# Optimization experiments

Hardware: AMD Instinct MI355X
Metric: run time of the kernel (lower is better)

The kernel has to match this reference:

```python
import jax, jax.numpy as jnp
import numpy as np

B, T, SD, AD, H, K, HID = 256, 128, 8, 2, 3, 4, 256


def setup_inputs() -> dict:
    key = jax.random.key(0)
    ks = jax.random.split(key, 12)
    inp = {
        "state": jax.random.normal(ks[0], (B, T, SD), dtype=jnp.float32),
        "action": jax.random.normal(ks[1], (B, T, AD), dtype=jnp.float32),
        # Linear(4, 4*H, bias=False): weight (4*H, 4)
        "Wk": jax.random.normal(ks[2], (4 * H, K), dtype=jnp.float32) * 0.1,
        "Wq": jax.random.normal(ks[3], (4 * H, SD + AD), dtype=jnp.float32) * 0.1,
        "Wv": jax.random.normal(ks[4], (4 * H, K), dtype=jnp.float32) * 0.1,
        # MLP: in_dim = 4*H + SD + AD -> HID -> HID -> 1
        "W1": jax.random.normal(ks[5], (HID, 4 * H + SD + AD), dtype=jnp.float32) * 0.05,
        "b1": jnp.zeros((HID,), dtype=jnp.float32),
        "W2": jax.random.normal(ks[6], (HID, HID), dtype=jnp.float32) * 0.05,
        "b2": jnp.zeros((HID,), dtype=jnp.float32),
        "Wout": jax.random.uniform(ks[7], (1, HID), minval=-0.003, maxval=0.003, dtype=jnp.float32),
        "bout": jax.random.uniform(ks[8], (1,), minval=-0.003, maxval=0.003, dtype=jnp.float32),
    }
    return inp


def reference(state, action, Wk, Wq, Wv, W1, b1, W2, b2, Wout, bout):
    q_state = jnp.concatenate([state, action], axis=-1)  # (b, t, sd+ad)
    s = state[:, :, :4]                                   # (b, t, 4)
    b, t, k = s.shape
    h = Wk.shape[0] // k
    # rel_full[b, i, j] = s[b, j] - s[b, i]  (matches torch view/transpose)
    rel_full = s[:, None, :, :] - s[:, :, None, :]        # (b, t, t, 4)
    # drop diagonal (self-pairs): idx[i] = all j != i, in order
    j = jnp.arange(t - 1)
    idx = j[None, :] + (j[None, :] >= jnp.arange(t)[:, None])  # (t, t-1)
    rel = jnp.take_along_axis(rel_full, idx[None, :, :, None], axis=2)  # (b, t, t-1, 4)
    # QKV projections (tiny head dim k=4)
    q = (q_state @ Wq.T).reshape(b, t, h, k)              # (b, t, h, 4)
    keys = (rel @ Wk.T).reshape(b, t, t - 1, h, k)        # (b, t, t-1, h, 4)
    vals = (rel @ Wv.T).reshape(b, t, t - 1, h, k)
    scores = jnp.einsum('bthk,btjhk->bthj', q, keys) / jnp.sqrt(jnp.float32(k))
    w = jax.nn.softmax(scores, axis=-1)                   # over the t-1 neighbors
    x = jnp.einsum('bthj,btjhk->bthk', w, vals).reshape(b, t, h * k)
    x = jnp.concatenate([x, q_state], axis=-1)            # (b, t, h*4 + sd+ad)
    x = jax.nn.relu(x @ W1.T + b1)
    x = jax.nn.relu(x @ W2.T + b2)
    return x @ Wout.T + bout                              # (b, t, 1)
```

## Files before the change

### kernel.cpp

```cpp
#include <hip/hip_runtime.h>
#include <math.h>

#define Bp 256
#define Tp 128
#define SDp 8
#define ADp 2
#define Hp 3
#define Kp 4
#define HIDp 256
#define QDp (SDp + ADp)
#define X1Dp (Hp * Kp + QDp)
#define X1PAD 32
#define H1LD 264
#define LOG2E 1.4426950408889634f

typedef short bf16x8 __attribute__((ext_vector_type(8)));
typedef float f32x4  __attribute__((ext_vector_type(4)));

__device__ __forceinline__ unsigned short f2bf(float f) {
    unsigned u = __float_as_uint(f);
    unsigned r = (u + 0x7FFFu + ((u >> 16) & 1u)) >> 16;
    return (unsigned short)r;
}

__global__ __launch_bounds__(256) void attn_prep_kernel(
    const float* __restrict__ state, const float* __restrict__ action,
    const float* __restrict__ Wk, const float* __restrict__ Wq,
    const float* __restrict__ Wv, const float* __restrict__ W1,
    const float* __restrict__ W2, unsigned short* __restrict__ W1b,
    unsigned short* __restrict__ W2b, unsigned short* __restrict__ X1b)
{
    if (blockIdx.x >= Bp) {
        const int id0 = (blockIdx.x - Bp) * 1024 + threadIdx.x * 4;
        if (id0 < HIDp * HIDp) {
            const float4 v = *(const float4*)(W2 + id0);
            ushort4 o;
            o.x = f2bf(v.x); o.y = f2bf(v.y); o.z = f2bf(v.z); o.w = f2bf(v.w);
            *(ushort4*)(W2b + id0) = o;
        } else {
            #pragma unroll
            for (int u = 0; u < 4; ++u) {
                const int i = id0 - HIDp * HIDp + u;
                const int r = i >> 5, k = i & 31;
                W1b[i] = (k < X1Dp) ? f2bf(W1[r * X1Dp + k]) : (unsigned short)0;
            }
        }
        return;
    }

    const int b  = blockIdx.x;
    const int t  = threadIdx.x & 127;
    const int jh = threadIdx.x >> 7;

    __shared__ float4 s4[Tp];
    __shared__ float  wq[Hp * Kp * QDp];
    __shared__ float  wk[Hp * Kp * Kp];
    __shared__ float  wv[Hp * Kp * Kp];
    __shared__ float  part[Tp][16];

    if (threadIdx.x < Tp)
        s4[threadIdx.x] = ((const float4*)(state + (size_t)b * Tp * SDp))[threadIdx.x * 2];
    if (threadIdx.x >= Tp && threadIdx.x < Tp + Hp * Kp * QDp)
        wq[threadIdx.x - Tp] = Wq[threadIdx.x - Tp];
    if (threadIdx.x < Hp * Kp * Kp) { wk[threadIdx.x] = Wk[threadIdx.x]; wv[threadIdx.x] = Wv[threadIdx.x]; }
    __syncthreads();

    float qs[QDp];
    {
        const float* srow = state + ((size_t)b * Tp + t) * SDp;
        #pragma unroll
        for (int d = 0; d < SDp; ++d) qs[d] = srow[d];
        const float* arow = action + ((size_t)b * Tp + t) * ADp;
        qs[8] = arow[0]; qs[9] = arow[1];
    }

    float q[Hp * Kp];
    #pragma unroll
    for (int r = 0; r < Hp * Kp; ++r) {
        float a = 0.f;
        #pragma unroll
        for (int d = 0; d < QDp; ++d) a += qs[d] * wq[r * QDp + d];
        q[r] = a;
    }
    float qkp[Hp * Kp];
    #pragma unroll
    for (int h = 0; h < Hp; ++h)
        #pragma unroll
        for (int c = 0; c < Kp; ++c) {
            float a = 0.f;
            #pragma unroll
            for (int k = 0; k < Kp; ++k) a += q[h * Kp + k] * wk[(h * Kp + k) * Kp + c];
            qkp[h * Kp + c] = 0.5f * LOG2E * a;
        }

    const float4 st = s4[t];
    float ch[Hp];
    #pragma unroll
    for (int h = 0; h < Hp; ++h)
        ch[h] = st.x * qkp[h*4] + st.y * qkp[h*4+1] + st.z * qkp[h*4+2] + st.w * qkp[h*4+3];

    float l[Hp] = {0.f, 0.f, 0.f};
    float accs[Hp][4] = {};
    const int j0 = jh * 64;
    for (int j = j0; j < j0 + 64; ++j) {
        const float4 sj = s4[j];
        #pragma unroll
        for (int h = 0; h < Hp; ++h) {
            const float d = sj.x * qkp[h*4] + sj.y * qkp[h*4+1]
                          + sj.z * qkp[h*4+2] + sj.w * qkp[h*4+3] - ch[h];
            const float e = (j == t) ? 0.f : exp2f(d);
            l[h] += e;
            accs[h][0] += e * sj.x; accs[h][1] += e * sj.y;
            accs[h][2] += e * sj.z; accs[h][3] += e * sj.w;
        }
    }

    if (jh == 1) {
        #pragma unroll
        for (int h = 0; h < Hp; ++h) {
            part[t][h] = l[h];
            #pragma unroll
            for (int c = 0; c < Kp; ++c) part[t][3 + h * 4 + c] = accs[h][c];
        }
    }
    __syncthreads();

    if (jh == 0) {
        unsigned short rowb[X1PAD];
        #pragma unroll
        for (int h = 0; h < Hp; ++h) {
            const float lt = l[h] + part[t][h];
            const float inv = 1.f / lt;
            const float rb0 = (accs[h][0] + part[t][3 + h*4 + 0]) * inv - st.x;
            const float rb1 = (accs[h][1] + part[t][3 + h*4 + 1]) * inv - st.y;
            const float rb2 = (accs[h][2] + part[t][3 + h*4 + 2]) * inv - st.z;
            const float rb3 = (accs[h][3] + part[t][3 + h*4 + 3]) * inv - st.w;
            #pragma unroll
            for (int k = 0; k < Kp; ++k) {
                const int r = h * Kp + k;
                rowb[r] = f2bf(rb0 * wv[r*4] + rb1 * wv[r*4+1] + rb2 * wv[r*4+2] + rb3 * wv[r*4+3]);
            }
        }
        #pragma unroll
        for (int i = 0; i < QDp; ++i) rowb[Hp * Kp + i] = f2bf(qs[i]);
        #pragma unroll
        for (int i = X1Dp; i < X1PAD; ++i) rowb[i] = 0;

        uint4* dst = (uint4*)(X1b + ((size_t)b * Tp + t) * X1PAD);
        const uint4* srcv = (const uint4*)rowb;
        #pragma unroll
        for (int i = 0; i < 4; ++i) dst[i] = srcv[i];
    }
}

__global__ __launch_bounds__(256, 4) void mlp_kernel(
    const unsigned short* __restrict__ X1b, const unsigned short* __restrict__ W1b,
    const unsigned short* __restrict__ W2b,
    const float* __restrict__ b1, const float* __restrict__ b2,
    const float* __restrict__ Wout, const float* __restrict__ bout,
    float* __restrict__ out)
{
    const int tid  = threadIdx.x;
    const int lane = tid & 63;
    const int wave = tid >> 6;
    const int quad = lane >> 4;
    const int l16  = lane & 15;
    const int pos0 = blockIdx.x * 64;

    __shared__ __align__(16) unsigned short h1s[64 * H1LD];

    {
        const bf16x8 afr = *(const bf16x8*)&X1b[((size_t)pos0 + wave * 16 + l16) * X1PAD + quad * 8];
        for (int nt = 0; nt < 16; ++nt) {
            const bf16x8 bfr = *(const bf16x8*)&W1b[(nt * 16 + l16) * X1PAD + quad * 8];
            f32x4 acc = {0.f, 0.f, 0.f, 0.f};
            acc = __builtin_amdgcn_mfma_f32_16x16x32_bf16(afr, bfr, acc, 0, 0, 0);
            const int col = nt * 16 + l16;
            const float bb = b1[col];
            #pragma unroll
            for (int r = 0; r < 4; ++r)
                h1s[(wave * 16 + quad * 4 + r) * H1LD + col] = f2bf(fmaxf(acc[r] + bb, 0.f));
        }
    }
    __syncthreads();

    bf16x8 A[8];
    #pragma unroll
    for (int ks = 0; ks < 8; ++ks)
        A[ks] = *(const bf16x8*)&h1s[(wave * 16 + l16) * H1LD + ks * 32 + quad * 8];

    float rsum[4] = {0.f, 0.f, 0.f, 0.f};
    for (int nt = 0; nt < 16; ++nt) {
        const int col = nt * 16 + l16;
        const unsigned short* wrow = W2b + (size_t)col * HIDp + quad * 8;
        bf16x8 Bf[8];
        #pragma unroll
        for (int ks = 0; ks < 8; ++ks)
            Bf[ks] = *(const bf16x8*)(wrow + ks * 32);
        f32x4 acc = {0.f, 0.f, 0.f, 0.f};
        #pragma unroll
        for (int ks = 0; ks < 8; ++ks)
            acc = __builtin_amdgcn_mfma_f32_16x16x32_bf16(A[ks], Bf[ks], acc, 0, 0, 0);
        const float bb = b2[col];
        const float wo = Wout[col];
        #pragma unroll
        for (int r = 0; r < 4; ++r)
            rsum[r] += fmaxf(acc[r] + bb, 0.f) * wo;
    }

    #pragma unroll
    for (int off = 1; off < 16; off <<= 1)
        #pragma unroll
        for (int r = 0; r < 4; ++r)
            rsum[r] += __shfl_xor(rsum[r], off, 64);

    if (l16 == 0) {
        const float bo = bout[0];
        #pragma unroll
        for (int r = 0; r < 4; ++r)
            out[pos0 + wave * 16 + quad * 4 + r] = rsum[r] + bo;
    }
}

extern "C" void kernel_launch(void* const* d_in, const int* in_sizes, int n_in,
                              void* d_out, int out_size, void* d_ws, size_t ws_size,
                              hipStream_t stream) {
    const float* state  = (const float*)d_in[0];
    const float* action = (const float*)d_in[1];
    const float* Wk     = (const float*)d_in[2];
    const float* Wq     = (const float*)d_in[3];
    const float* Wv     = (const float*)d_in[4];
    const float* W1     = (const float*)d_in[5];
    const float* b1     = (const float*)d_in[6];
    const float* W2     = (const float*)d_in[7];
    const float* b2     = (const float*)d_in[8];
    const float* Wout   = (const float*)d_in[9];
    const float* bout   = (const float*)d_in[10];
    float* out = (float*)d_out;

    char* ws = (char*)d_ws;
    unsigned short* W1b = (unsigned short*)(ws);
    unsigned short* W2b = (unsigned short*)(ws + 16384);
    unsigned short* X1b = (unsigned short*)(ws + 16384 + 131072);

    attn_prep_kernel<<<Bp + 72, 256, 0, stream>>>(state, action, Wk, Wq, Wv, W1, W2,
                                                  W1b, W2b, X1b);
    mlp_kernel<<<(Bp * Tp) / 64, 256, 0, stream>>>(X1b, W1b, W2b, b1, b2, Wout, bout, out);
}
```

Measured before the change: 121.0 us.

## Fuse attention prep and MLP into one kernel with LDS-staged weights

Merges the attention-prep and MLP kernels into a single 512-thread kernel, one block per batch element. The attention output and the bf16 W1 now stay in LDS instead of going through a global workspace, and the neighbour loop is split across four thread groups instead of two. Each block converts W2 to bf16 and stages it through LDS in two halves, replacing the per-wave global loads of W2. The cost is redundant W2 conversion in every block and about 135KB of LDS per block, which limits occupancy to one block per CU.

```diff
diff --git a/kernel.cpp b/kernel.cpp
--- a/kernel.cpp
+++ b/kernel.cpp
@@ -10,7 +10,8 @@
 #define HIDp 256
 #define QDp (SDp + ADp)
 #define X1Dp (Hp * Kp + QDp)
-#define X1PAD 32
+#define X1LD 40
+#define W1LD 40
 #define H1LD 264
 #define LOG2E 1.4426950408889634f
 
@@ -23,46 +24,53 @@
     return (unsigned short)r;
 }
 
-__global__ __launch_bounds__(256) void attn_prep_kernel(
+__global__ __launch_bounds__(512, 2) void fused_kernel(
     const float* __restrict__ state, const float* __restrict__ action,
     const float* __restrict__ Wk, const float* __restrict__ Wq,
     const float* __restrict__ Wv, const float* __restrict__ W1,
-    const float* __restrict__ W2, unsigned short* __restrict__ W1b,
-    unsigned short* __restrict__ W2b, unsigned short* __restrict__ X1b)
+    const float* __restrict__ b1, const float* __restrict__ W2,
+    const float* __restrict__ b2, const float* __restrict__ Wout,
+    const float* __restrict__ bout, float* __restrict__ out)
 {
-    if (blockIdx.x >= Bp) {
-        const int id0 = (blockIdx.x - Bp) * 1024 + threadIdx.x * 4;
-        if (id0 < HIDp * HIDp) {
-            const float4 v = *(const float4*)(W2 + id0);
-            ushort4 o;
-            o.x = f2bf(v.x); o.y = f2bf(v.y); o.z = f2bf(v.z); o.w = f2bf(v.w);
-            *(ushort4*)(W2b + id0) = o;
-        } else {
-            #pragma unroll
-            for (int u = 0; u < 4; ++u) {
-                const int i = id0 - HIDp * HIDp + u;
-                const int r = i >> 5, k = i & 31;
-                W1b[i] = (k < X1Dp) ? f2bf(W1[r * X1Dp + k]) : (unsigned short)0;
-            }
-        }
-        return;
-    }
-
-    const int b  = blockIdx.x;
-    const int t  = threadIdx.x & 127;
-    const int jh = threadIdx.x >> 7;
-
-    __shared__ float4 s4[Tp];
-    __shared__ float  wq[Hp * Kp * QDp];
-    __shared__ float  wk[Hp * Kp * Kp];
-    __shared__ float  wv[Hp * Kp * Kp];
-    __shared__ float  part[Tp][16];
-
-    if (threadIdx.x < Tp)
-        s4[threadIdx.x] = ((const float4*)(state + (size_t)b * Tp * SDp))[threadIdx.x * 2];
-    if (threadIdx.x >= Tp && threadIdx.x < Tp + Hp * Kp * QDp)
-        wq[threadIdx.x - Tp] = Wq[threadIdx.x - Tp];
-    if (threadIdx.x < Hp * Kp * Kp) { wk[threadIdx.x] = Wk[threadIdx.x]; wv[threadIdx.x] = Wv[threadIdx.x]; }
+    __shared__ __align__(16) char lds[135168];
+    unsigned short* h1s = (unsigned short*)lds;
+    char* R2 = lds + 67584;
+    float*  part = (float*)(R2);
+    float4* s4   = (float4*)(R2 + 26112);
+    float*  wq   = (float*)(R2 + 28160);
+    float*  wk   = (float*)(R2 + 28640);
+    float*  wv   = (float*)(R2 + 28832);
+    unsigned short* W1s = (unsigned short*)(R2 + 29024);
+    unsigned short* X1s = (unsigned short*)(R2 + 49504);
+    unsigned short* W2s = (unsigned short*)(R2);
+
+    const int b    = blockIdx.x;
+    const int tid  = threadIdx.x;
+    const int t    = tid & 127;
+    const int jh   = tid >> 7;
+    const int lane = tid & 63;
+    const int wave = tid >> 6;
+    const int quad = lane >> 4;
+    const int l16  = lane & 15;
+
+    if (tid < Tp) {
+        s4[tid] = ((const float4*)(state + (size_t)b * Tp * SDp))[tid * 2];
+    } else if (tid < Tp + 120) {
+        wq[tid - Tp] = Wq[tid - Tp];
+    } else if (tid < Tp + 168) {
+        wk[tid - Tp - 120] = Wk[tid - Tp - 120];
+    } else if (tid < Tp + 216) {
+        wv[tid - Tp - 168] = Wv[tid - Tp - 168];
+    }
+    {
+        const int row = tid >> 1, c0 = (tid & 1) * 16;
+        const float* wr = W1 + row * X1Dp;
+        #pragma unroll
+        for (int i = 0; i < 16; ++i) {
+            const int c = c0 + i;
+            W1s[row * W1LD + c] = (c < X1Dp) ? f2bf(wr[c]) : (unsigned short)0;
+        }
+    }
     __syncthreads();
 
     float qs[QDp];
@@ -94,20 +102,20 @@
         }
 
     const float4 st = s4[t];
-    float ch[Hp];
+    float ch0[Hp];
     #pragma unroll
     for (int h = 0; h < Hp; ++h)
-        ch[h] = st.x * qkp[h*4] + st.y * qkp[h*4+1] + st.z * qkp[h*4+2] + st.w * qkp[h*4+3];
+        ch0[h] = st.x * qkp[h*4] + st.y * qkp[h*4+1] + st.z * qkp[h*4+2] + st.w * qkp[h*4+3];
 
     float l[Hp] = {0.f, 0.f, 0.f};
     float accs[Hp][4] = {};
-    const int j0 = jh * 64;
-    for (int j = j0; j < j0 + 64; ++j) {
+    const int j0 = jh * 32;
+    for (int j = j0; j < j0 + 32; ++j) {
         const float4 sj = s4[j];
         #pragma unroll
         for (int h = 0; h < Hp; ++h) {
             const float d = sj.x * qkp[h*4] + sj.y * qkp[h*4+1]
-                          + sj.z * qkp[h*4+2] + sj.w * qkp[h*4+3] - ch[h];
+                          + sj.z * qkp[h*4+2] + sj.w * qkp[h*4+3] - ch0[h];
             const float e = (j == t) ? 0.f : exp2f(d);
             l[h] += e;
             accs[h][0] += e * sj.x; accs[h][1] += e * sj.y;
@@ -115,26 +123,35 @@
         }
     }
 
-    if (jh == 1) {
+    if (jh > 0) {
+        float* pp = part + ((jh - 1) * 128 + t) * 17;
         #pragma unroll
         for (int h = 0; h < Hp; ++h) {
-            part[t][h] = l[h];
-            #pragma unroll
-            for (int c = 0; c < Kp; ++c) part[t][3 + h * 4 + c] = accs[h][c];
+            pp[h] = l[h];
+            #pragma unroll
+            for (int c = 0; c < Kp; ++c) pp[3 + h * 4 + c] = accs[h][c];
         }
     }
     __syncthreads();
 
     if (jh == 0) {
-        unsigned short rowb[X1PAD];
+        unsigned short rowb[32] __attribute__((aligned(16)));
         #pragma unroll
         for (int h = 0; h < Hp; ++h) {
-            const float lt = l[h] + part[t][h];
+            float lt = l[h];
+            float a0 = accs[h][0], a1 = accs[h][1], a2 = accs[h][2], a3 = accs[h][3];
+            #pragma unroll
+            for (int p = 0; p < 3; ++p) {
+                const float* pp = part + (p * 128 + t) * 17;
+                lt += pp[h];
+                a0 += pp[3 + h*4 + 0]; a1 += pp[3 + h*4 + 1];
+                a2 += pp[3 + h*4 + 2]; a3 += pp[3 + h*4 + 3];
+            }
             const float inv = 1.f / lt;
-            const float rb0 = (accs[h][0] + part[t][3 + h*4 + 0]) * inv - st.x;
-            const float rb1 = (accs[h][1] + part[t][3 + h*4 + 1]) * inv - st.y;
-            const float rb2 = (accs[h][2] + part[t][3 + h*4 + 2]) * inv - st.z;
-            const float rb3 = (accs[h][3] + part[t][3 + h*4 + 3]) * inv - st.w;
+            const float rb0 = a0 * inv - st.x;
+            const float rb1 = a1 * inv - st.y;
+            const float rb2 = a2 * inv - st.z;
+            const float rb3 = a3 * inv - st.w;
             #pragma unroll
             for (int k = 0; k < Kp; ++k) {
                 const int r = h * Kp + k;
@@ -144,35 +161,19 @@
         #pragma unroll
         for (int i = 0; i < QDp; ++i) rowb[Hp * Kp + i] = f2bf(qs[i]);
         #pragma unroll
-        for (int i = X1Dp; i < X1PAD; ++i) rowb[i] = 0;
-
-        uint4* dst = (uint4*)(X1b + ((size_t)b * Tp + t) * X1PAD);
+        for (int i = X1Dp; i < 32; ++i) rowb[i] = 0;
+
+        uint4* dst = (uint4*)(X1s + t * X1LD);
         const uint4* srcv = (const uint4*)rowb;
         #pragma unroll
         for (int i = 0; i < 4; ++i) dst[i] = srcv[i];
     }
-}
-
-__global__ __launch_bounds__(256, 4) void mlp_kernel(
-    const unsigned short* __restrict__ X1b, const unsigned short* __restrict__ W1b,
-    const unsigned short* __restrict__ W2b,
-    const float* __restrict__ b1, const float* __restrict__ b2,
-    const float* __restrict__ Wout, const float* __restrict__ bout,
-    float* __restrict__ out)
-{
-    const int tid  = threadIdx.x;
-    const int lane = tid & 63;
-    const int wave = tid >> 6;
-    const int quad = lane >> 4;
-    const int l16  = lane & 15;
-    const int pos0 = blockIdx.x * 64;
-
-    __shared__ __align__(16) unsigned short h1s[64 * H1LD];
+    __syncthreads();
 
     {
-        const bf16x8 afr = *(const bf16x8*)&X1b[((size_t)pos0 + wave * 16 + l16) * X1PAD + quad * 8];
+        const bf16x8 afr = *(const bf16x8*)&X1s[(wave * 16 + l16) * X1LD + quad * 8];
         for (int nt = 0; nt < 16; ++nt) {
-            const bf16x8 bfr = *(const bf16x8*)&W1b[(nt * 16 + l16) * X1PAD + quad * 8];
+            const bf16x8 bfr = *(const bf16x8*)&W1s[(nt * 16 + l16) * W1LD + quad * 8];
             f32x4 acc = {0.f, 0.f, 0.f, 0.f};
             acc = __builtin_amdgcn_mfma_f32_16x16x32_bf16(afr, bfr, acc, 0, 0, 0);
             const int col = nt * 16 + l16;
@@ -190,22 +191,36 @@
         A[ks] = *(const bf16x8*)&h1s[(wave * 16 + l16) * H1LD + ks * 32 + quad * 8];
 
     float rsum[4] = {0.f, 0.f, 0.f, 0.f};
-    for (int nt = 0; nt < 16; ++nt) {
-        const int col = nt * 16 + l16;
-        const unsigned short* wrow = W2b + (size_t)col * HIDp + quad * 8;
-        bf16x8 Bf[8];
-        #pragma unroll
-        for (int ks = 0; ks < 8; ++ks)
-            Bf[ks] = *(const bf16x8*)(wrow + ks * 32);
-        f32x4 acc = {0.f, 0.f, 0.f, 0.f};
-        #pragma unroll
-        for (int ks = 0; ks < 8; ++ks)
-            acc = __builtin_amdgcn_mfma_f32_16x16x32_bf16(A[ks], Bf[ks], acc, 0, 0, 0);
-        const float bb = b2[col];
-        const float wo = Wout[col];
-        #pragma unroll
-        for (int r = 0; r < 4; ++r)
-            rsum[r] += fmaxf(acc[r] + bb, 0.f) * wo;
+    const int srow8 = tid >> 6;
+    const int c4    = tid & 63;
+    #pragma unroll
+    for (int chh = 0; chh < 2; ++chh) {
+        if (chh) __syncthreads();
+        #pragma unroll
+        for (int pass = 0; pass < 16; ++pass) {
+            const int r_loc = pass * 8 + srow8;
+            const float4 v = *(const float4*)(W2 + ((size_t)(chh * 128 + r_loc)) * HIDp + c4 * 4);
+            ushort4 o;
+            o.x = f2bf(v.x); o.y = f2bf(v.y); o.z = f2bf(v.z); o.w = f2bf(v.w);
+            *(ushort4*)&W2s[r_loc * H1LD + c4 * 4] = o;
+        }
+        __syncthreads();
+        for (int nt = 0; nt < 8; ++nt) {
+            const int col = chh * 128 + nt * 16 + l16;
+            bf16x8 Bf[8];
+            #pragma unroll
+            for (int ks = 0; ks < 8; ++ks)
+                Bf[ks] = *(const bf16x8*)&W2s[(nt * 16 + l16) * H1LD + ks * 32 + quad * 8];
+            f32x4 acc = {0.f, 0.f, 0.f, 0.f};
+            #pragma unroll
+            for (int ks = 0; ks < 8; ++ks)
+                acc = __builtin_amdgcn_mfma_f32_16x16x32_bf16(A[ks], Bf[ks], acc, 0, 0, 0);
+            const float bb = b2[col];
+            const float wo = Wout[col];
+            #pragma unroll
+            for (int r = 0; r < 4; ++r)
+                rsum[r] += fmaxf(acc[r] + bb, 0.f) * wo;
+        }
     }
 
     #pragma unroll
@@ -218,7 +233,7 @@
         const float bo = bout[0];
         #pragma unroll
         for (int r = 0; r < 4; ++r)
-            out[pos0 + wave * 16 + quad * 4 + r] = rsum[r] + bo;
+            out[(size_t)b * Tp + wave * 16 + quad * 4 + r] = rsum[r] + bo;
     }
 }
 
@@ -238,12 +253,8 @@
     const float* bout   = (const float*)d_in[10];
     float* out = (float*)d_out;
 
-    char* ws = (char*)d_ws;
-    unsigned short* W1b = (unsigned short*)(ws);
-    unsigned short* W2b = (unsigned short*)(ws + 16384);
-    unsigned short* X1b = (unsigned short*)(ws + 16384 + 131072);
-
-    attn_prep_kernel<<<Bp + 72, 256, 0, stream>>>(state, action, Wk, Wq, Wv, W1, W2,
-                                                  W1b, W2b, X1b);
-    mlp_kernel<<<(Bp * Tp) / 64, 256, 0, stream>>>(X1b, W1b, W2b, b1, b2, Wout, bout, out);
+    (void)d_ws; (void)ws_size;
+
+    fused_kernel<<<Bp, 512, 0, stream>>>(state, action, Wk, Wq, Wv, W1, b1,
+                                         W2, b2, Wout, bout, out);
 }
```

Result: faster. 114.5 us (-5.4%).

## Fuse attention and MLP into one kernel with XOR-swizzled LDS and N-split layer two

Applied to the files above, without the earlier changes.

Merges the attention and MLP kernels so X1 stays in LDS and never goes through global memory. Weight conversion moves into a separate small prep kernel. Each block now handles 64 positions of one batch row, with the 128-key loop split across the four quads and combined by shuffles. Layer two is split by output columns per wave, so each W2 tile loaded from global is reused across four row tiles. The h1 buffer uses an XOR swizzle to avoid LDS bank conflicts. The cost is more registers (A[4][8]), fewer blocks (512), and the attention phase now running in the same kernel as the MFMA work.

```diff
diff --git a/kernel.cpp b/kernel.cpp
--- a/kernel.cpp
+++ b/kernel.cpp
@@ -10,8 +10,7 @@
 #define HIDp 256
 #define QDp (SDp + ADp)
 #define X1Dp (Hp * Kp + QDp)
-#define X1PAD 32
-#define H1LD 264
+#define X1LD 40
 #define LOG2E 1.4426950408889634f
 
 typedef short bf16x8 __attribute__((ext_vector_type(8)));
@@ -23,54 +22,70 @@
     return (unsigned short)r;
 }
 
-__global__ __launch_bounds__(256) void attn_prep_kernel(
+__device__ __forceinline__ unsigned h1_byte(int row, int col2bytes) {
+    unsigned off = ((unsigned)row << 9) + (unsigned)col2bytes;
+    return off ^ ((unsigned)(row & 7) << 4);
+}
+
+__global__ __launch_bounds__(256) void prep_kernel(
+    const float* __restrict__ W1, const float* __restrict__ W2,
+    unsigned short* __restrict__ W1b, unsigned short* __restrict__ W2b)
+{
+    const int bid = blockIdx.x;
+    if (bid < 64) {
+        const int i = (bid * 256 + threadIdx.x) * 4;
+        const float4 v = *(const float4*)(W2 + i);
+        ushort4 o;
+        o.x = f2bf(v.x); o.y = f2bf(v.y); o.z = f2bf(v.z); o.w = f2bf(v.w);
+        *(ushort4*)(W2b + i) = o;
+    } else {
+        const int i = (bid - 64) * 256 + threadIdx.x;
+        const int r = i >> 5, c = i & 31;
+        W1b[i] = (c < X1Dp) ? f2bf(W1[r * X1Dp + c]) : (unsigned short)0;
+    }
+}
+
+__global__ __launch_bounds__(256, 2) void main_kernel(
     const float* __restrict__ state, const float* __restrict__ action,
     const float* __restrict__ Wk, const float* __restrict__ Wq,
-    const float* __restrict__ Wv, const float* __restrict__ W1,
-    const float* __restrict__ W2, unsigned short* __restrict__ W1b,
-    unsigned short* __restrict__ W2b, unsigned short* __restrict__ X1b)
+    const float* __restrict__ Wv,
+    const unsigned short* __restrict__ W1b, const unsigned short* __restrict__ W2b,
+    const float* __restrict__ b1, const float* __restrict__ b2,
+    const float* __restrict__ Wout, const float* __restrict__ bout,
+    float* __restrict__ out)
 {
-    if (blockIdx.x >= Bp) {
-        const int id0 = (blockIdx.x - Bp) * 1024 + threadIdx.x * 4;
-        if (id0 < HIDp * HIDp) {
-            const float4 v = *(const float4*)(W2 + id0);
-            ushort4 o;
-            o.x = f2bf(v.x); o.y = f2bf(v.y); o.z = f2bf(v.z); o.w = f2bf(v.w);
-            *(ushort4*)(W2b + id0) = o;
-        } else {
-            #pragma unroll
-            for (int u = 0; u < 4; ++u) {
-                const int i = id0 - HIDp * HIDp + u;
-                const int r = i >> 5, k = i & 31;
-                W1b[i] = (k < X1Dp) ? f2bf(W1[r * X1Dp + k]) : (unsigned short)0;
-            }
-        }
-        return;
-    }
-
-    const int b  = blockIdx.x;
-    const int t  = threadIdx.x & 127;
-    const int jh = threadIdx.x >> 7;
+    const int bid   = blockIdx.x;
+    const int batch = bid >> 1;
+    const int t0    = (bid & 1) * 64;
+    const int tid   = threadIdx.x;
+    const int lane  = tid & 63;
+    const int wave  = tid >> 6;
+    const int l16   = lane & 15;
+    const int quad  = lane >> 4;
+    const int pos   = wave * 16 + l16;
+    const int t     = t0 + pos;
 
     __shared__ float4 s4[Tp];
     __shared__ float  wq[Hp * Kp * QDp];
     __shared__ float  wk[Hp * Kp * Kp];
     __shared__ float  wv[Hp * Kp * Kp];
-    __shared__ float  part[Tp][16];
-
-    if (threadIdx.x < Tp)
-        s4[threadIdx.x] = ((const float4*)(state + (size_t)b * Tp * SDp))[threadIdx.x * 2];
-    if (threadIdx.x >= Tp && threadIdx.x < Tp + Hp * Kp * QDp)
-        wq[threadIdx.x - Tp] = Wq[threadIdx.x - Tp];
-    if (threadIdx.x < Hp * Kp * Kp) { wk[threadIdx.x] = Wk[threadIdx.x]; wv[threadIdx.x] = Wv[threadIdx.x]; }
+    __shared__ __align__(16) unsigned short X1s[64 * X1LD];
+    __shared__ __align__(16) unsigned short h1s[64 * 256];
+    __shared__ __align__(16) float partial[4][64];
+
+    if (tid < Tp)
+        s4[tid] = ((const float4*)(state + (size_t)batch * Tp * SDp))[tid * 2];
+    if (tid >= Tp && tid < Tp + Hp * Kp * QDp)
+        wq[tid - Tp] = Wq[tid - Tp];
+    if (tid < Hp * Kp * Kp) { wk[tid] = Wk[tid]; wv[tid] = Wv[tid]; }
     __syncthreads();
 
     float qs[QDp];
     {
-        const float* srow = state + ((size_t)b * Tp + t) * SDp;
+        const float* srow = state + ((size_t)batch * Tp + t) * SDp;
         #pragma unroll
         for (int d = 0; d < SDp; ++d) qs[d] = srow[d];
-        const float* arow = action + ((size_t)b * Tp + t) * ADp;
+        const float* arow = action + ((size_t)batch * Tp + t) * ADp;
         qs[8] = arow[0]; qs[9] = arow[1];
     }
 
@@ -94,131 +109,138 @@
         }
 
     const float4 st = s4[t];
-    float ch[Hp];
+    float ch0[Hp];
     #pragma unroll
     for (int h = 0; h < Hp; ++h)
-        ch[h] = st.x * qkp[h*4] + st.y * qkp[h*4+1] + st.z * qkp[h*4+2] + st.w * qkp[h*4+3];
+        ch0[h] = st.x * qkp[h*4] + st.y * qkp[h*4+1] + st.z * qkp[h*4+2] + st.w * qkp[h*4+3];
 
     float l[Hp] = {0.f, 0.f, 0.f};
     float accs[Hp][4] = {};
-    const int j0 = jh * 64;
-    for (int j = j0; j < j0 + 64; ++j) {
+    const int j0 = quad * 32;
+    for (int j = j0; j < j0 + 32; ++j) {
         const float4 sj = s4[j];
         #pragma unroll
         for (int h = 0; h < Hp; ++h) {
             const float d = sj.x * qkp[h*4] + sj.y * qkp[h*4+1]
-                          + sj.z * qkp[h*4+2] + sj.w * qkp[h*4+3] - ch[h];
+                          + sj.z * qkp[h*4+2] + sj.w * qkp[h*4+3] - ch0[h];
             const float e = (j == t) ? 0.f : exp2f(d);
             l[h] += e;
             accs[h][0] += e * sj.x; accs[h][1] += e * sj.y;
             accs[h][2] += e * sj.z; accs[h][3] += e * sj.w;
         }
     }
-
-    if (jh == 1) {
-        #pragma unroll
-        for (int h = 0; h < Hp; ++h) {
-            part[t][h] = l[h];
-            #pragma unroll
-            for (int c = 0; c < Kp; ++c) part[t][3 + h * 4 + c] = accs[h][c];
-        }
-    }
-    __syncthreads();
-
-    if (jh == 0) {
-        unsigned short rowb[X1PAD];
-        #pragma unroll
-        for (int h = 0; h < Hp; ++h) {
-            const float lt = l[h] + part[t][h];
-            const float inv = 1.f / lt;
-            const float rb0 = (accs[h][0] + part[t][3 + h*4 + 0]) * inv - st.x;
-            const float rb1 = (accs[h][1] + part[t][3 + h*4 + 1]) * inv - st.y;
-            const float rb2 = (accs[h][2] + part[t][3 + h*4 + 2]) * inv - st.z;
-            const float rb3 = (accs[h][3] + part[t][3 + h*4 + 3]) * inv - st.w;
-            #pragma unroll
-            for (int k = 0; k < Kp; ++k) {
-                const int r = h * Kp + k;
-                rowb[r] = f2bf(rb0 * wv[r*4] + rb1 * wv[r*4+1] + rb2 * wv[r*4+2] + rb3 * wv[r*4+3]);
-            }
-        }
-        #pragma unroll
-        for (int i = 0; i < QDp; ++i) rowb[Hp * Kp + i] = f2bf(qs[i]);
-        #pragma unroll
-        for (int i = X1Dp; i < X1PAD; ++i) rowb[i] = 0;
-
-        uint4* dst = (uint4*)(X1b + ((size_t)b * Tp + t) * X1PAD);
-        const uint4* srcv = (const uint4*)rowb;
-        #pragma unroll
-        for (int i = 0; i < 4; ++i) dst[i] = srcv[i];
-    }
-}
-
-__global__ __launch_bounds__(256, 4) void mlp_kernel(
-    const unsigned short* __restrict__ X1b, const unsigned short* __restrict__ W1b,
-    const unsigned short* __restrict__ W2b,
-    const float* __restrict__ b1, const float* __restrict__ b2,
-    const float* __restrict__ Wout, const float* __restrict__ bout,
-    float* __restrict__ out)
-{
-    const int tid  = threadIdx.x;
-    const int lane = tid & 63;
-    const int wave = tid >> 6;
-    const int quad = lane >> 4;
-    const int l16  = lane & 15;
-    const int pos0 = blockIdx.x * 64;
-
-    __shared__ __align__(16) unsigned short h1s[64 * H1LD];
+    #pragma unroll
+    for (int h = 0; h < Hp; ++h) {
+        l[h] += __shfl_xor(l[h], 16); l[h] += __shfl_xor(l[h], 32);
+        #pragma unroll
+        for (int c = 0; c < Kp; ++c) {
+            accs[h][c] += __shfl_xor(accs[h][c], 16);
+            accs[h][c] += __shfl_xor(accs[h][c], 32);
+        }
+    }
+
+    if (quad < Hp) {
+        const int h = quad;
+        const float inv = 1.f / l[h];
+        const float rb0 = accs[h][0] * inv - st.x;
+        const float rb1 = accs[h][1] * inv - st.y;
+        const float rb2 = accs[h][2] * inv - st.z;
+        const float rb3 = accs[h][3] * inv - st.w;
+        ushort4 o;
+        {
+            const int r0 = h * Kp;
+            o.x = f2bf(rb0*wv[(r0+0)*4] + rb1*wv[(r0+0)*4+1] + rb2*wv[(r0+0)*4+2] + rb3*wv[(r0+0)*4+3]);
+            o.y = f2bf(rb0*wv[(r0+1)*4] + rb1*wv[(r0+1)*4+1] + rb2*wv[(r0+1)*4+2] + rb3*wv[(r0+1)*4+3]);
+            o.z = f2bf(rb0*wv[(r0+2)*4] + rb1*wv[(r0+2)*4+1] + rb2*wv[(r0+2)*4+2] + rb3*wv[(r0+2)*4+3]);
+            o.w = f2bf(rb0*wv[(r0+3)*4] + rb1*wv[(r0+3)*4+1] + rb2*wv[(r0+3)*4+2] + rb3*wv[(r0+3)*4+3]);
+        }
+        *(ushort4*)&X1s[pos * X1LD + h * 4] = o;
+    } else {
+        uint2 d[5];
+        d[0].x = (unsigned)f2bf(qs[0]) | ((unsigned)f2bf(qs[1]) << 16);
+        d[0].y = (unsigned)f2bf(qs[2]) | ((unsigned)f2bf(qs[3]) << 16);
+        d[1].x = (unsigned)f2bf(qs[4]) | ((unsigned)f2bf(qs[5]) << 16);
+        d[1].y = (unsigned)f2bf(qs[6]) | ((unsigned)f2bf(qs[7]) << 16);
+        d[2].x = (unsigned)f2bf(qs[8]) | ((unsigned)f2bf(qs[9]) << 16);
+        d[2].y = 0u; d[3].x = 0u; d[3].y = 0u; d[4].x = 0u; d[4].y = 0u;
+        uint2* dst = (uint2*)&X1s[pos * X1LD + 12];
+        #pragma unroll
+        for (int i = 0; i < 5; ++i) dst[i] = d[i];
+    }
+    __syncthreads();
 
     {
-        const bf16x8 afr = *(const bf16x8*)&X1b[((size_t)pos0 + wave * 16 + l16) * X1PAD + quad * 8];
+        const bf16x8 afr = *(const bf16x8*)&X1s[pos * X1LD + quad * 8];
         for (int nt = 0; nt < 16; ++nt) {
-            const bf16x8 bfr = *(const bf16x8*)&W1b[(nt * 16 + l16) * X1PAD + quad * 8];
+            const bf16x8 bfr = *(const bf16x8*)&W1b[(nt * 16 + l16) * 32 + quad * 8];
             f32x4 acc = {0.f, 0.f, 0.f, 0.f};
             acc = __builtin_amdgcn_mfma_f32_16x16x32_bf16(afr, bfr, acc, 0, 0, 0);
             const int col = nt * 16 + l16;
             const float bb = b1[col];
             #pragma unroll
-            for (int r = 0; r < 4; ++r)
-                h1s[(wave * 16 + quad * 4 + r) * H1LD + col] = f2bf(fmaxf(acc[r] + bb, 0.f));
-        }
-    }
-    __syncthreads();
-
-    bf16x8 A[8];
-    #pragma unroll
-    for (int ks = 0; ks < 8; ++ks)
-        A[ks] = *(const bf16x8*)&h1s[(wave * 16 + l16) * H1LD + ks * 32 + quad * 8];
-
-    float rsum[4] = {0.f, 0.f, 0.f, 0.f};
-    for (int nt = 0; nt < 16; ++nt) {
+            for (int r = 0; r < 4; ++r) {
+                const int row = wave * 16 + quad * 4 + r;
+                *(unsigned short*)((char*)h1s + h1_byte(row, col * 2)) =
+                    f2bf(fmaxf(acc[r] + bb, 0.f));
+            }
+        }
+    }
+    __syncthreads();
+
+    bf16x8 A[4][8];
+    #pragma unroll
+    for (int rt = 0; rt < 4; ++rt)
+        #pragma unroll
+        for (int ks = 0; ks < 8; ++ks) {
+            const int row = rt * 16 + l16;
+            A[rt][ks] = *(const bf16x8*)((const char*)h1s + h1_byte(row, ks * 64 + quad * 16));
+        }
+
+    float rsum[4][4] = {};
+    #pragma unroll 1
+    for (int i = 0; i < 4; ++i) {
+        const int nt  = wave * 4 + i;
         const int col = nt * 16 + l16;
-        const unsigned short* wrow = W2b + (size_t)col * HIDp + quad * 8;
+        const unsigned short* wr = W2b + (size_t)col * HIDp + quad * 8;
         bf16x8 Bf[8];
         #pragma unroll
         for (int ks = 0; ks < 8; ++ks)
-            Bf[ks] = *(const bf16x8*)(wrow + ks * 32);
-        f32x4 acc = {0.f, 0.f, 0.f, 0.f};
-        #pragma unroll
-        for (int ks = 0; ks < 8; ++ks)
-            acc = __builtin_amdgcn_mfma_f32_16x16x32_bf16(A[ks], Bf[ks], acc, 0, 0, 0);
+            Bf[ks] = *(const bf16x8*)(wr + ks * 32);
         const float bb = b2[col];
         const float wo = Wout[col];
         #pragma unroll
-        for (int r = 0; r < 4; ++r)
-            rsum[r] += fmaxf(acc[r] + bb, 0.f) * wo;
+        for (int rt = 0; rt < 4; ++rt) {
+            f32x4 acc = {0.f, 0.f, 0.f, 0.f};
+            #pragma unroll
+            for (int ks = 0; ks < 8; ++ks)
+                acc = __builtin_amdgcn_mfma_f32_16x16x32_bf16(A[rt][ks], Bf[ks], acc, 0, 0, 0);
+            #pragma unroll
+            for (int r = 0; r < 4; ++r)
+                rsum[rt][r] += fmaxf(acc[r] + bb, 0.f) * wo;
+        }
     }
 
     #pragma unroll
     for (int off = 1; off < 16; off <<= 1)
         #pragma unroll
-        for (int r = 0; r < 4; ++r)
-            rsum[r] += __shfl_xor(rsum[r], off, 64);
+        for (int rt = 0; rt < 4; ++rt)
+            #pragma unroll
+            for (int r = 0; r < 4; ++r)
+                rsum[rt][r] += __shfl_xor(rsum[rt][r], off);
 
     if (l16 == 0) {
-        const float bo = bout[0];
-        #pragma unroll
-        for (int r = 0; r < 4; ++r)
-            out[pos0 + wave * 16 + quad * 4 + r] = rsum[r] + bo;
+        #pragma unroll
+        for (int rt = 0; rt < 4; ++rt) {
+            f32x4 v = {rsum[rt][0], rsum[rt][1], rsum[rt][2], rsum[rt][3]};
+            *(f32x4*)&partial[wave][rt * 16 + quad * 4] = v;
+        }
+    }
+    __syncthreads();
+
+    if (tid < 64) {
+        const float o = partial[0][tid] + partial[1][tid] + partial[2][tid]
+                      + partial[3][tid] + bout[0];
+        out[(size_t)batch * Tp + t0 + tid] = o;
     }
 }
 
@@ -241,9 +263,8 @@
     char* ws = (char*)d_ws;
     unsigned short* W1b = (unsigned short*)(ws);
     unsigned short* W2b = (unsigned short*)(ws + 16384);
-    unsigned short* X1b = (unsigned short*)(ws + 16384 + 131072);
-
-    attn_prep_kernel<<<Bp + 72, 256, 0, stream>>>(state, action, Wk, Wq, Wv, W1, W2,
-                                                  W1b, W2b, X1b);
-    mlp_kernel<<<(Bp * Tp) / 64, 256, 0, stream>>>(X1b, W1b, W2b, b1, b2, Wout, bout, out);
-}
+
+    prep_kernel<<<96, 256, 0, stream>>>(W1, W2, W1b, W2b);
+    main_kernel<<<2 * Bp, 256, 0, stream>>>(state, action, Wk, Wq, Wv,
+                                            W1b, W2b, b1, b2, Wout, bout, out);
+}
```

Measured after the change: 120.1 us. Within noise of the previous version (-0.7%).
